# Performance work log

Hardware: AMD Instinct MI355X
Metric: run time of the kernel (lower is better)

## Reference

```python
import jax, jax.numpy as jnp
import numpy as np

NUM_USERS = 50000
NUM_ITEMS = 50000
N_NODES = NUM_USERS + NUM_ITEMS
DIM_FEAT = 256
HID = 128
EMB = 128
K = 3
N_EDGES = 1_600_000


def setup_inputs() -> dict:
    key = jax.random.key(0)
    ks = jax.random.split(key, 16)

    def xavier(k, shape):
        fan_in, fan_out = shape[-2], shape[-1]
        std = float(np.sqrt(2.0 / (fan_in + fan_out)))
        return jax.random.normal(k, shape, dtype=jnp.float32) * std

    return {
        "feat": jax.random.normal(ks[0], (NUM_ITEMS, DIM_FEAT), dtype=jnp.float32),
        "node_emb": jax.random.normal(ks[1], (N_NODES, EMB), dtype=jnp.float32),
        "src": jax.random.randint(ks[2], (N_EDGES,), 0, N_NODES, dtype=jnp.int32),
        "dst": jax.random.randint(ks[3], (N_EDGES,), 0, N_NODES, dtype=jnp.int32),
        "user_feat_emb": xavier(ks[4], (NUM_USERS, HID)),
        "trans_w": xavier(ks[5], (DIM_FEAT, HID)),
        "trans_b": jnp.zeros((HID,), dtype=jnp.float32),
        # layer 0: hidden->hidden; layers 1,2: emb->emb. hidden==emb so stack.
        "ws": xavier(ks[6], (K, HID, HID)),
        "des_w": xavier(ks[7], (K, HID, EMB)),
        "des_b": jnp.zeros((K, EMB), dtype=jnp.float32),
        # concat=True: outs[i] takes [h | u] of width hidden+emb
        "out_w": xavier(ks[8], (K, HID + EMB, EMB)),
        "out_b": jnp.zeros((K, EMB), dtype=jnp.float32),
    }


def reference(feat, node_emb, src, dst, user_feat_emb,
              trans_w, trans_b, ws, des_w, des_b, out_w, out_b):
    # feat = trans(feat); concat user embeddings; L2-normalize rows
    x = feat @ trans_w + trans_b                      # [num_items, HID]
    x = jnp.concatenate([user_feat_emb, x], axis=0)   # [N, HID]
    norm = jnp.linalg.norm(x, axis=1, keepdims=True)
    x = x / jnp.maximum(norm, 1e-12)

    lrelu = jax.nn.leaky_relu  # slope 0.01, matches F.leaky_relu default
    for i in range(K):
        # g.func(x, W): sparse adjacency aggregation (sum over in-edges) then dense W
        agg = jax.ops.segment_sum(x[src], dst, num_segments=N_NODES)  # [N, HID]
        h = lrelu(agg @ ws[i])                                        # [N, HID]
        u = lrelu(h @ des_w[i] + des_b[i] + node_emb)                 # [N, EMB]
        x = lrelu(jnp.concatenate([h, u], axis=1) @ out_w[i] + out_b[i])
    return x, user_feat_emb
```

## Files before the change

### kernel.cpp

```cpp
#include <hip/hip_runtime.h>

#define NN 100000
#define NU 50000
#define NI 50000
#define NE 1600000
#define NSLICE 3
#define SLICEW 33334

#define HSLICE 4
#define HCHUNK 64
#define HSW 25600
#define HEPC (NE/HCHUNK)

typedef unsigned short u16;
typedef unsigned int u32;

typedef __attribute__((ext_vector_type(8))) short s16x8;
typedef __attribute__((ext_vector_type(4))) float f32x4;
typedef __attribute__((ext_vector_type(4))) unsigned short us4;

__device__ __forceinline__ float bf2f(u16 u){
  union { u32 i; float f; } v; v.i = ((u32)u) << 16; return v.f;
}
__device__ __forceinline__ u16 f2bf(float f){
  union { float f; u32 i; } v; v.f = f;
  u32 u = v.i;
  return (u16)((u + 0x7FFFu + ((u >> 16) & 1u)) >> 16);
}
__device__ __forceinline__ u32 pack2(float lo, float hi){
  return (u32)f2bf(lo) | ((u32)f2bf(hi) << 16);
}
__device__ __forceinline__ float lrelu(float x){ return x > 0.f ? x : 0.01f * x; }
__device__ __forceinline__ float san(float v){
  union { float f; u32 i; } u; u.f = v;
  return ((u.i & 0x7F800000u) == 0x7F800000u) ? 0.f : v;
}

__global__ __launch_bounds__(256) void transpose_weights(
    const float* __restrict__ trans_w, const float* __restrict__ wsw,
    const float* __restrict__ desw, const float* __restrict__ outw,
    u16* __restrict__ Ttw, u16* __restrict__ Tw, u16* __restrict__ Td, u16* __restrict__ To)
{
  __shared__ u16 L[128][136];
  int b = blockIdx.x, t = threadIdx.x;
  const float* src; u16* dst; int stride;
  if (b < 2)      { src = trans_w + b*16384;        dst = Ttw + b*128;          stride = 256; }
  else if (b < 5) { int i = b-2; src = wsw  + i*16384; dst = Tw + i*16384;      stride = 128; }
  else if (b < 8) { int i = b-5; src = desw + i*16384; dst = Td + i*16384;      stride = 128; }
  else            { int i = (b-8)>>1, h = (b-8)&1;
                    src = outw + i*32768 + h*16384;    dst = To + i*32768 + h*128; stride = 256; }
  #pragma unroll
  for (int p = 0; p < 8; p++){
    int fi = (p*256 + t)*8;
    int r = fi >> 7, c = fi & 127;
    f32x4 v0 = *(const f32x4*)(src + r*128 + c);
    f32x4 v1 = *(const f32x4*)(src + r*128 + c + 4);
    L[c+0][r] = f2bf(san(v0.x)); L[c+1][r] = f2bf(san(v0.y));
    L[c+2][r] = f2bf(san(v0.z)); L[c+3][r] = f2bf(san(v0.w));
    L[c+4][r] = f2bf(san(v1.x)); L[c+5][r] = f2bf(san(v1.y));
    L[c+6][r] = f2bf(san(v1.z)); L[c+7][r] = f2bf(san(v1.w));
  }
  __syncthreads();
  #pragma unroll
  for (int p = 0; p < 8; p++){
    int fi = (p*256 + t)*8;
    int n = fi >> 7, k = fi & 127;
    us4 o0, o1;
    o0.x = L[n][k+0]; o0.y = L[n][k+1]; o0.z = L[n][k+2]; o0.w = L[n][k+3];
    o1.x = L[n][k+4]; o1.y = L[n][k+5]; o1.z = L[n][k+6]; o1.w = L[n][k+7];
    *(us4*)(dst + (size_t)n*stride + k)     = o0;
    *(us4*)(dst + (size_t)n*stride + k + 4) = o1;
  }
}

__global__ __launch_bounds__(256) void conv_nemb(
    const float* __restrict__ nemb, u16* __restrict__ nembB)
{
  int i = blockIdx.x*256 + threadIdx.x;
  size_t off = (size_t)i * 8;
  f32x4 v0 = *(const f32x4*)(nemb + off);
  f32x4 v1 = *(const f32x4*)(nemb + off + 4);
  us4 o0, o1;
  o0.x = f2bf(san(v0.x)); o0.y = f2bf(san(v0.y)); o0.z = f2bf(san(v0.z)); o0.w = f2bf(san(v0.w));
  o1.x = f2bf(san(v1.x)); o1.y = f2bf(san(v1.y)); o1.z = f2bf(san(v1.z)); o1.w = f2bf(san(v1.w));
  *(us4*)(nembB + off)     = o0;
  *(us4*)(nembB + off + 4) = o1;
}

__global__ __launch_bounds__(256) void norm_users(const float* __restrict__ ufe, u16* __restrict__ X)
{
  int gid = blockIdx.x*256 + threadIdx.x;
  int row = gid >> 6, lane = gid & 63;
  float2 v = *(const float2*)(ufe + (size_t)row*128 + lane*2);
  float a = san(v.x), b = san(v.y);
  float ss = a*a + b*b;
  #pragma unroll
  for (int off = 32; off; off >>= 1) ss += __shfl_xor(ss, off, 64);
  float inv = 1.0f / fmaxf(sqrtf(ss), 1e-12f);
  *(u32*)(X + (size_t)row*128 + lane*2) = pack2(a*inv, b*inv);
}

__global__ __launch_bounds__(256, 4) void trans_items(
    const float* __restrict__ feat, const u16* __restrict__ Ttw,
    const float* __restrict__ tb, u16* __restrict__ X)
{
  __shared__ u16 Af[64][136];
  __shared__ float rowss[64][8];
  __shared__ float rnorm[64];

  int t = threadIdx.x;
  int r0 = blockIdx.x * 64;
  int w = t >> 6, lane = t & 63;
  int l15 = lane & 15, q = lane >> 4;
  int m0 = (w & 1) * 64, n0 = (w >> 1) * 32;

  f32x4 acc[4][2];
  #pragma unroll
  for (int mi = 0; mi < 4; mi++)
    #pragma unroll
    for (int ni = 0; ni < 2; ni++){ acc[mi][ni].x = 0.f; acc[mi][ni].y = 0.f; acc[mi][ni].z = 0.f; acc[mi][ni].w = 0.f; }

  for (int half = 0; half < 2; half++){
    __syncthreads();
    #pragma unroll
    for (int p = 0; p < 4; p++){
      int fi = (p*256 + t)*8;
      int r = fi >> 7, c = fi & 127;
      int row = r0 + r;
      us4 o0 = {0,0,0,0}, o1 = {0,0,0,0};
      if (row < NI){
        f32x4 v0 = *(const f32x4*)(feat + (size_t)row*256 + half*128 + c);
        f32x4 v1 = *(const f32x4*)(feat + (size_t)row*256 + half*128 + c + 4);
        o0.x = f2bf(san(v0.x)); o0.y = f2bf(san(v0.y)); o0.z = f2bf(san(v0.z)); o0.w = f2bf(san(v0.w));
        o1.x = f2bf(san(v1.x)); o1.y = f2bf(san(v1.y)); o1.z = f2bf(san(v1.z)); o1.w = f2bf(san(v1.w));
      }
      *(us4*)&Af[r][c]     = o0;
      *(us4*)&Af[r][c + 4] = o1;
    }
    __syncthreads();
    #pragma unroll
    for (int kc = 0; kc < 128; kc += 32){
      s16x8 afr[4], bfr[2];
      #pragma unroll
      for (int mi = 0; mi < 4; mi++)
        afr[mi] = *(const s16x8*)(Ttw + (size_t)(m0 + 16*mi + l15)*256 + half*128 + kc + 8*q);
      #pragma unroll
      for (int ni = 0; ni < 2; ni++) bfr[ni] = *(const s16x8*)&Af[n0 + 16*ni + l15][kc + 8*q];
      #pragma unroll
      for (int mi = 0; mi < 4; mi++)
        #pragma unroll
        for (int ni = 0; ni < 2; ni++)
          acc[mi][ni] = __builtin_amdgcn_mfma_f32_16x16x32_bf16(afr[mi], bfr[ni], acc[mi][ni], 0, 0, 0);
    }
  }

  float bias[4][4];
  #pragma unroll
  for (int mi = 0; mi < 4; mi++){
    int c0 = m0 + 16*mi + 4*q;
    f32x4 bv = *(const f32x4*)(tb + c0);
    bias[mi][0] = san(bv.x); bias[mi][1] = san(bv.y); bias[mi][2] = san(bv.z); bias[mi][3] = san(bv.w);
  }
  #pragma unroll
  for (int ni = 0; ni < 2; ni++){
    float ss = 0.f;
    #pragma unroll
    for (int mi = 0; mi < 4; mi++){
      float v0 = acc[mi][ni].x + bias[mi][0];
      float v1 = acc[mi][ni].y + bias[mi][1];
      float v2 = acc[mi][ni].z + bias[mi][2];
      float v3 = acc[mi][ni].w + bias[mi][3];
      ss += v0*v0 + v1*v1 + v2*v2 + v3*v3;
    }
    rowss[n0 + 16*ni + l15][(w & 1)*4 + q] = ss;
  }
  __syncthreads();
  if (t < 64){
    float s = 0.f;
    #pragma unroll
    for (int j = 0; j < 8; j++) s += rowss[t][j];
    rnorm[t] = 1.0f / fmaxf(sqrtf(s), 1e-12f);
  }
  __syncthreads();
  #pragma unroll
  for (int mi = 0; mi < 4; mi++){
    int c0 = m0 + 16*mi + 4*q;
    #pragma unroll
    for (int ni = 0; ni < 2; ni++){
      int r = n0 + 16*ni + l15;
      int row = r0 + r;
      if (row < NI){
        float inv = rnorm[r];
        us4 o;
        o.x = f2bf((acc[mi][ni].x + bias[mi][0]) * inv);
        o.y = f2bf((acc[mi][ni].y + bias[mi][1]) * inv);
        o.z = f2bf((acc[mi][ni].z + bias[mi][2]) * inv);
        o.w = f2bf((acc[mi][ni].w + bias[mi][3]) * inv);
        *(us4*)(X + (size_t)(NU + row)*128 + c0) = o;
      }
    }
  }
}

__global__ __launch_bounds__(1024) void hist_lds(
    const int* __restrict__ dst, u32* __restrict__ countsC)
{
  __shared__ u32 cnt[HSW];
  int b = blockIdx.x;
  int s = b / HCHUNK, c = b % HCHUNK;
  int t = threadIdx.x;
  for (int i = t; i < HSW; i += 1024) cnt[i] = 0;
  __syncthreads();
  int lo = s * HSW;
  int hi = min(lo + HSW, NN);
  int e0 = c * HEPC, e1 = e0 + HEPC;
  for (int e = e0 + t*4; e < e1; e += 4096){
    int4 d4 = *(const int4*)(dst + e);
    int d0 = min(max(d4.x, 0), NN-1);
    int d1 = min(max(d4.y, 0), NN-1);
    int d2 = min(max(d4.z, 0), NN-1);
    int d3 = min(max(d4.w, 0), NN-1);
    if (d0 >= lo && d0 < hi) atomicAdd(&cnt[d0 - lo], 1u);
    if (d1 >= lo && d1 < hi) atomicAdd(&cnt[d1 - lo], 1u);
    if (d2 >= lo && d2 < hi) atomicAdd(&cnt[d2 - lo], 1u);
    if (d3 >= lo && d3 < hi) atomicAdd(&cnt[d3 - lo], 1u);
  }
  __syncthreads();
  u32* outp = countsC + (size_t)c*NN + lo;
  int w = hi - lo;
  for (int i = t; i < w; i += 1024) outp[i] = cnt[i];
}

__global__ __launch_bounds__(256) void reduce_counts(
    const u32* __restrict__ countsC, int* __restrict__ counts)
{
  int v = blockIdx.x*256 + threadIdx.x;
  if (v < NN){
    u32 sum = 0;
    #pragma unroll
    for (int c = 0; c < HCHUNK; c++) sum += countsC[(size_t)c*NN + v];
    counts[v] = (int)sum;
  }
}

__global__ __launch_bounds__(1024) void scan_k(const int* __restrict__ counts, int* __restrict__ row_ptr){
  __shared__ int wsum[16];
  __shared__ int woff[16];
  __shared__ int tot;
  int t = threadIdx.x;
  int lane = t & 63, wid = t >> 6;
  int carry = 0;
  for (int base = 0; base < NN; base += 4096){
    int idx = base + t*4;
    int4 v = {0,0,0,0};
    if (idx < NN) v = *(const int4*)(counts + idx);
    int s4 = v.x + v.y + v.z + v.w;
    int s = s4;
    #pragma unroll
    for (int off = 1; off < 64; off <<= 1){
      int u = __shfl_up(s, off, 64);
      if (lane >= off) s += u;
    }
    if (lane == 63) wsum[wid] = s;
    __syncthreads();
    if (t < 16){
      int ws = wsum[t];
      int wscan = ws;
      #pragma unroll
      for (int off = 1; off < 16; off <<= 1){
        int u = __shfl_up(wscan, off, 64);
        if (t >= off) wscan += u;
      }
      woff[t] = wscan - ws;
      if (t == 15) tot = wscan;
    }
    __syncthreads();
    if (idx < NN){
      int e0 = carry + woff[wid] + (s - s4);
      int4 o;
      o.x = e0; o.y = e0 + v.x; o.z = o.y + v.y; o.w = o.z + v.z;
      *(int4*)(row_ptr + idx) = o;
    }
    carry += tot;
    __syncthreads();
  }
}

__global__ __launch_bounds__(256) void fill_slice(
    const int* __restrict__ src, const int* __restrict__ dst,
    int* __restrict__ row_ptr, int* __restrict__ esrc, int d0, int d1)
{
  int e = blockIdx.x*256 + threadIdx.x;
  if (e < NE){
    int d = dst[e];
    if (d >= d0 && d < d1){
      d = min(max(d, 0), NN - 1);
      int pos = atomicAdd(&row_ptr[d], 1);
      pos = min(max(pos, 0), NE - 1);
      esrc[pos] = src[e];
    }
  }
}

#define ACC8(P) \
  a0 += bf2f((u16)(P.x & 0xFFFF)); a1 += bf2f((u16)(P.x >> 16)); \
  a2 += bf2f((u16)(P.y & 0xFFFF)); a3 += bf2f((u16)(P.y >> 16)); \
  a4 += bf2f((u16)(P.z & 0xFFFF)); a5 += bf2f((u16)(P.z >> 16)); \
  a6 += bf2f((u16)(P.w & 0xFFFF)); a7 += bf2f((u16)(P.w >> 16));

__global__ __launch_bounds__(256) void aggregate(
    const u16* __restrict__ X, const int* __restrict__ row_ptr,
    const int* __restrict__ esrc, u16* __restrict__ AGG)
{
  int gid = blockIdx.x*256 + threadIdx.x;
  int v = gid >> 6, lane = gid & 63;
  int sub = lane >> 4, li = lane & 15;
  int jb = (v == 0) ? 0 : row_ptr[v - 1];
  int je = row_ptr[v];
  jb = min(max(jb, 0), NE);
  je = min(max(je, jb), NE);

  float a0=0.f,a1=0.f,a2=0.f,a3=0.f,a4=0.f,a5=0.f,a6=0.f,a7=0.f;

  int j = jb + sub;
  for (; j + 12 < je; j += 16){
    int s0 = esrc[j];      s0 = min(max(s0, 0), NN - 1);
    int s1 = esrc[j + 4];  s1 = min(max(s1, 0), NN - 1);
    int s2 = esrc[j + 8];  s2 = min(max(s2, 0), NN - 1);
    int s3 = esrc[j + 12]; s3 = min(max(s3, 0), NN - 1);
    uint4 p0 = *(const uint4*)(X + (size_t)s0*128 + li*8);
    uint4 p1 = *(const uint4*)(X + (size_t)s1*128 + li*8);
    uint4 p2 = *(const uint4*)(X + (size_t)s2*128 + li*8);
    uint4 p3 = *(const uint4*)(X + (size_t)s3*128 + li*8);
    ACC8(p0); ACC8(p1); ACC8(p2); ACC8(p3);
  }
  for (; j + 4 < je; j += 8){
    int s0 = esrc[j];     s0 = min(max(s0, 0), NN - 1);
    int s1 = esrc[j + 4]; s1 = min(max(s1, 0), NN - 1);
    uint4 p0 = *(const uint4*)(X + (size_t)s0*128 + li*8);
    uint4 p1 = *(const uint4*)(X + (size_t)s1*128 + li*8);
    ACC8(p0); ACC8(p1);
  }
  for (; j < je; j += 4){
    int s0 = esrc[j]; s0 = min(max(s0, 0), NN - 1);
    uint4 p0 = *(const uint4*)(X + (size_t)s0*128 + li*8);
    ACC8(p0);
  }

  a0 += __shfl_xor(a0, 16, 64); a0 += __shfl_xor(a0, 32, 64);
  a1 += __shfl_xor(a1, 16, 64); a1 += __shfl_xor(a1, 32, 64);
  a2 += __shfl_xor(a2, 16, 64); a2 += __shfl_xor(a2, 32, 64);
  a3 += __shfl_xor(a3, 16, 64); a3 += __shfl_xor(a3, 32, 64);
  a4 += __shfl_xor(a4, 16, 64); a4 += __shfl_xor(a4, 32, 64);
  a5 += __shfl_xor(a5, 16, 64); a5 += __shfl_xor(a5, 32, 64);
  a6 += __shfl_xor(a6, 16, 64); a6 += __shfl_xor(a6, 32, 64);
  a7 += __shfl_xor(a7, 16, 64); a7 += __shfl_xor(a7, 32, 64);

  if (sub == 0){
    uint4 o;
    o.x = pack2(a0, a1); o.y = pack2(a2, a3);
    o.z = pack2(a4, a5); o.w = pack2(a6, a7);
    *(uint4*)(AGG + (size_t)v*128 + li*8) = o;
  }
}

__global__ __launch_bounds__(256, 2) void layer_fused(
    const u16* __restrict__ AGG, const u16* __restrict__ nembB,
    const u16* __restrict__ Twi, const u16* __restrict__ Tdi,
    const float* __restrict__ dbF, const u16* __restrict__ Toi,
    const float* __restrict__ obF, u16* __restrict__ XoutB,
    float* __restrict__ XoutF, int last)
{
  __shared__ u16 Ab[128][136];
  __shared__ u16 Hb[128][136];

  int t = threadIdx.x;
  int r0 = blockIdx.x * 128;
  int w = t >> 6, lane = t & 63;
  int l15 = lane & 15, q = lane >> 4;
  int m0 = (w & 1) * 64, n0 = (w >> 1) * 64;

  f32x4 acc[4][4];
  s16x8 wa[4][4], wb[4][4];

#define ZERO_ACC() \
  { _Pragma("unroll") for (int mi = 0; mi < 4; mi++) \
      { _Pragma("unroll") for (int ni = 0; ni < 4; ni++) \
        { acc[mi][ni].x = 0.f; acc[mi][ni].y = 0.f; acc[mi][ni].z = 0.f; acc[mi][ni].w = 0.f; } } }

#define LOADW(WF, WBASE, WSTRIDE, WKOFF) \
  { _Pragma("unroll") for (int mi = 0; mi < 4; mi++) \
      { _Pragma("unroll") for (int kk = 0; kk < 4; kk++) \
          WF[mi][kk] = *(const s16x8*)((WBASE) + (size_t)(m0 + 16*mi + l15)*(WSTRIDE) + (WKOFF) + kk*32 + 8*q); } }

#define MFMA_PHASE(BARR, WF) \
  { _Pragma("unroll") for (int kk = 0; kk < 4; kk++){ \
      s16x8 bfr[4]; \
      _Pragma("unroll") for (int ni = 0; ni < 4; ni++) bfr[ni] = *(const s16x8*)&BARR[n0 + 16*ni + l15][kk*32 + 8*q]; \
      _Pragma("unroll") for (int mi = 0; mi < 4; mi++) \
        { _Pragma("unroll") for (int ni = 0; ni < 4; ni++) \
          acc[mi][ni] = __builtin_amdgcn_mfma_f32_16x16x32_bf16(WF[mi][kk], bfr[ni], acc[mi][ni], 0, 0, 0); } } }

  LOADW(wa, Twi, 128, 0);

  #pragma unroll
  for (int p = 0; p < 8; p++){
    int fi = (p*256 + t)*8;
    int r = fi >> 7, c = fi & 127;
    int row = r0 + r;
    us4 o0 = {0,0,0,0}, o1 = {0,0,0,0};
    if (row < NN){
      o0 = *(const us4*)(AGG + (size_t)row*128 + c);
      o1 = *(const us4*)(AGG + (size_t)row*128 + c + 4);
    }
    *(us4*)&Ab[r][c]     = o0;
    *(us4*)&Ab[r][c + 4] = o1;
  }
  __syncthreads();

  ZERO_ACC();
  LOADW(wb, Tdi, 128, 0);
  MFMA_PHASE(Ab, wa);

  #pragma unroll
  for (int mi = 0; mi < 4; mi++){
    #pragma unroll
    for (int ni = 0; ni < 4; ni++){
      us4 o;
      o.x = f2bf(lrelu(acc[mi][ni].x));
      o.y = f2bf(lrelu(acc[mi][ni].y));
      o.z = f2bf(lrelu(acc[mi][ni].z));
      o.w = f2bf(lrelu(acc[mi][ni].w));
      *(us4*)&Hb[n0 + 16*ni + l15][m0 + 16*mi + 4*q] = o;
    }
  }
  __syncthreads();

  ZERO_ACC();
  LOADW(wa, Toi, 256, 0);
  MFMA_PHASE(Hb, wb);

  #pragma unroll
  for (int mi = 0; mi < 4; mi++){
    int c0 = m0 + 16*mi + 4*q;
    f32x4 dbv = *(const f32x4*)(dbF + c0);
    float db0 = san(dbv.x), db1 = san(dbv.y), db2 = san(dbv.z), db3 = san(dbv.w);
    #pragma unroll
    for (int ni = 0; ni < 4; ni++){
      int r = n0 + 16*ni + l15;
      int row = r0 + r;
      float e0 = 0.f, e1 = 0.f, e2 = 0.f, e3 = 0.f;
      if (row < NN){
        us4 ne = *(const us4*)(nembB + (size_t)row*128 + c0);
        e0 = bf2f(ne.x); e1 = bf2f(ne.y); e2 = bf2f(ne.z); e3 = bf2f(ne.w);
      }
      us4 o;
      o.x = f2bf(lrelu(acc[mi][ni].x + db0 + e0));
      o.y = f2bf(lrelu(acc[mi][ni].y + db1 + e1));
      o.z = f2bf(lrelu(acc[mi][ni].z + db2 + e2));
      o.w = f2bf(lrelu(acc[mi][ni].w + db3 + e3));
      *(us4*)&Ab[r][c0] = o;
    }
  }
  __syncthreads();

  ZERO_ACC();
  LOADW(wb, Toi, 256, 128);
  MFMA_PHASE(Hb, wa);
  MFMA_PHASE(Ab, wb);

  #pragma unroll
  for (int mi = 0; mi < 4; mi++){
    int c0 = m0 + 16*mi + 4*q;
    f32x4 obv = *(const f32x4*)(obF + c0);
    float b0 = san(obv.x), b1 = san(obv.y), b2 = san(obv.z), b3 = san(obv.w);
    #pragma unroll
    for (int ni = 0; ni < 4; ni++){
      int r = n0 + 16*ni + l15;
      int row = r0 + r;
      if (row < NN){
        if (last){
          f32x4 o;
          o.x = lrelu(acc[mi][ni].x + b0);
          o.y = lrelu(acc[mi][ni].y + b1);
          o.z = lrelu(acc[mi][ni].z + b2);
          o.w = lrelu(acc[mi][ni].w + b3);
          *(f32x4*)(XoutF + (size_t)row*128 + c0) = o;
        } else {
          us4 o;
          o.x = f2bf(lrelu(acc[mi][ni].x + b0));
          o.y = f2bf(lrelu(acc[mi][ni].y + b1));
          o.z = f2bf(lrelu(acc[mi][ni].z + b2));
          o.w = f2bf(lrelu(acc[mi][ni].w + b3));
          *(us4*)(XoutB + (size_t)row*128 + c0) = o;
        }
      }
    }
  }
#undef ZERO_ACC
#undef LOADW
#undef MFMA_PHASE
}

__global__ void copy_ufe(const float4* __restrict__ s, float4* __restrict__ d, int n){
  int i = blockIdx.x*256 + threadIdx.x;
  if (i < n){
    float4 v = s[i];
    v.x = san(v.x); v.y = san(v.y); v.z = san(v.z); v.w = san(v.w);
    d[i] = v;
  }
}

extern "C" void kernel_launch(void* const* d_in, const int* in_sizes, int n_in,
                              void* d_out, int out_size, void* d_ws, size_t ws_size,
                              hipStream_t stream)
{
  const float* feat = (const float*)d_in[0];
  const float* nemb = (const float*)d_in[1];
  const int*   src  = (const int*)d_in[2];
  const int*   dst  = (const int*)d_in[3];
  const float* ufe  = (const float*)d_in[4];
  const float* tw   = (const float*)d_in[5];
  const float* tb   = (const float*)d_in[6];
  const float* wsw  = (const float*)d_in[7];
  const float* desw = (const float*)d_in[8];
  const float* desb = (const float*)d_in[9];
  const float* outw = (const float*)d_in[10];
  const float* outb = (const float*)d_in[11];

  float* out  = (float*)d_out;
  float* outU = out + (size_t)NN*128;

  u16* X = (u16*)out;
  u16* nembB = (u16*)outU;

  char* p = (char*)d_ws;
  u16*   AGG = (u16*)p;    p += (size_t)NN*128*2;
  u16*   Ttw = (u16*)p;    p += (size_t)2*16384*2;
  u16*   Tw  = (u16*)p;    p += (size_t)3*16384*2;
  u16*   Td  = (u16*)p;    p += (size_t)3*16384*2;
  u16*   To  = (u16*)p;    p += (size_t)3*32768*2;
  int* row_ptr = (int*)p;  p += (size_t)100004*4;
  int* counts  = (int*)p;  p += (size_t)100000*4;
  int* esrc    = (int*)p;  p += (size_t)NE*4;
  u32* countsC = (u32*)AGG;

  transpose_weights<<<14, 256, 0, stream>>>(tw, wsw, desw, outw, Ttw, Tw, Td, To);
  conv_nemb<<<6250, 256, 0, stream>>>(nemb, nembB);
  norm_users<<<NU/4, 256, 0, stream>>>(ufe, X);
  trans_items<<<(NI + 63)/64, 256, 0, stream>>>(feat, Ttw, tb, X);

  hist_lds<<<HSLICE*HCHUNK, 1024, 0, stream>>>(dst, countsC);
  reduce_counts<<<(NN + 255)/256, 256, 0, stream>>>(countsC, counts);
  scan_k<<<1, 1024, 0, stream>>>(counts, row_ptr);
  for (int s = 0; s < NSLICE; s++){
    fill_slice<<<(NE + 255)/256, 256, 0, stream>>>(src, dst, row_ptr, esrc,
        s*SLICEW, (s == NSLICE-1) ? NN : (s+1)*SLICEW);
  }

  for (int i = 0; i < 3; i++){
    aggregate<<<NN/4, 256, 0, stream>>>(X, row_ptr, esrc, AGG);
    layer_fused<<<(NN + 127)/128, 256, 0, stream>>>(AGG, nembB,
        Tw + (size_t)i*16384, Td + (size_t)i*16384, desb + (size_t)i*128,
        To + (size_t)i*32768, outb + (size_t)i*128, X, out, (i == 2) ? 1 : 0);
  }
  copy_ufe<<<(NU*128/4 + 255)/256, 256, 0, stream>>>((const float4*)ufe, (float4*)outU, NU*128/4);
}
```

Baseline: 713.5 us.

## Fuse CSR gather aggregation into layer GEMM kernel for first two layers

Adds a layer_fused_agg kernel that gathers neighbour rows from the CSR edge list directly into shared memory, then runs the three chained GEMMs. This drops the separate aggregate kernel and the AGG round-trip through global memory for layers 0 and 1, ping-ponging X between buffers. The last layer keeps the separate aggregate path because its output buffer aliases the input. It also stops holding the weight fragments in registers across phases and reloads them per GEMM instead. The fused kernel may lose gather parallelism and latency hiding, since each 16-lane group walks 8 rows serially under a 2-blocks-per-SM launch bound.

```diff
diff --git a/kernel.cpp b/kernel.cpp
--- a/kernel.cpp
+++ b/kernel.cpp
@@ -364,44 +364,158 @@
   }
 }
 
-__global__ __launch_bounds__(256, 2) void layer_fused(
-    const u16* __restrict__ AGG, const u16* __restrict__ nembB,
+#define ZERO_ACC() \
+  { _Pragma("unroll") for (int mi = 0; mi < 4; mi++) \
+      { _Pragma("unroll") for (int ni = 0; ni < 4; ni++) \
+        { acc[mi][ni].x = 0.f; acc[mi][ni].y = 0.f; acc[mi][ni].z = 0.f; acc[mi][ni].w = 0.f; } } }
+
+#define GEMMG(BARR, WBASE, WSTRIDE, WKOFF) \
+  { s16x8 afr[4][4]; \
+    _Pragma("unroll") for (int mi = 0; mi < 4; mi++) \
+      { _Pragma("unroll") for (int kk = 0; kk < 4; kk++) \
+          afr[mi][kk] = *(const s16x8*)((WBASE) + (size_t)(m0 + 16*mi + l15)*(WSTRIDE) + (WKOFF) + kk*32 + 8*q); } \
+    _Pragma("unroll") for (int kk = 0; kk < 4; kk++){ \
+      s16x8 bfr[4]; \
+      _Pragma("unroll") for (int ni = 0; ni < 4; ni++) bfr[ni] = *(const s16x8*)&BARR[n0 + 16*ni + l15][kk*32 + 8*q]; \
+      _Pragma("unroll") for (int mi = 0; mi < 4; mi++) \
+        { _Pragma("unroll") for (int ni = 0; ni < 4; ni++) \
+          acc[mi][ni] = __builtin_amdgcn_mfma_f32_16x16x32_bf16(afr[mi][kk], bfr[ni], acc[mi][ni], 0, 0, 0); } } }
+
+#define LAYER_BODY(NEMBB, TWI, TDI, DBF, TOI, OBF, LAST_EXPR)                  \
+                                                \
+  ZERO_ACC();                                                                  \
+  GEMMG(Ab, TWI, 128, 0);                                                      \
+  _Pragma("unroll")                                                            \
+  for (int mi = 0; mi < 4; mi++){                                              \
+    _Pragma("unroll")                                                          \
+    for (int ni = 0; ni < 4; ni++){                                            \
+      us4 o;                                                                   \
+      o.x = f2bf(lrelu(acc[mi][ni].x));                                        \
+      o.y = f2bf(lrelu(acc[mi][ni].y));                                        \
+      o.z = f2bf(lrelu(acc[mi][ni].z));                                        \
+      o.w = f2bf(lrelu(acc[mi][ni].w));                                        \
+      *(us4*)&Hb[n0 + 16*ni + l15][m0 + 16*mi + 4*q] = o;                      \
+    }                                                                          \
+  }                                                                            \
+  __syncthreads();                                                             \
+                                                  \
+  ZERO_ACC();                                                                  \
+  GEMMG(Hb, TDI, 128, 0);                                                      \
+  _Pragma("unroll")                                                            \
+  for (int mi = 0; mi < 4; mi++){                                              \
+    int c0 = m0 + 16*mi + 4*q;                                                 \
+    f32x4 dbv = *(const f32x4*)(DBF + c0);                                     \
+    float db0 = san(dbv.x), db1 = san(dbv.y), db2 = san(dbv.z), db3 = san(dbv.w); \
+    _Pragma("unroll")                                                          \
+    for (int ni = 0; ni < 4; ni++){                                            \
+      int r = n0 + 16*ni + l15;                                                \
+      int row = r0 + r;                                                        \
+      float e0 = 0.f, e1 = 0.f, e2 = 0.f, e3 = 0.f;                            \
+      if (row < NN){                                                           \
+        us4 ne = *(const us4*)(NEMBB + (size_t)row*128 + c0);                  \
+        e0 = bf2f(ne.x); e1 = bf2f(ne.y); e2 = bf2f(ne.z); e3 = bf2f(ne.w);    \
+      }                                                                        \
+      us4 o;                                                                   \
+      o.x = f2bf(lrelu(acc[mi][ni].x + db0 + e0));                             \
+      o.y = f2bf(lrelu(acc[mi][ni].y + db1 + e1));                             \
+      o.z = f2bf(lrelu(acc[mi][ni].z + db2 + e2));                             \
+      o.w = f2bf(lrelu(acc[mi][ni].w + db3 + e3));                             \
+      *(us4*)&Ab[r][c0] = o;                                                   \
+    }                                                                          \
+  }                                                                            \
+  __syncthreads();                                                             \
+                       \
+  ZERO_ACC();                                                                  \
+  GEMMG(Hb, TOI, 256, 0);                                                      \
+  GEMMG(Ab, TOI, 256, 128);
+
+__global__ __launch_bounds__(256, 2) void layer_fused_agg(
+    const u16* __restrict__ Xin, const int* __restrict__ row_ptr,
+    const int* __restrict__ esrc, const u16* __restrict__ nembB,
     const u16* __restrict__ Twi, const u16* __restrict__ Tdi,
     const float* __restrict__ dbF, const u16* __restrict__ Toi,
-    const float* __restrict__ obF, u16* __restrict__ XoutB,
-    float* __restrict__ XoutF, int last)
-{
-  __shared__ u16 Ab[128][136];
-  __shared__ u16 Hb[128][136];
+    const float* __restrict__ obF, u16* __restrict__ XoutB)
+{
+  __shared__ __align__(16) u16 Ab[128][136];
+  __shared__ __align__(16) u16 Hb[128][136];
 
   int t = threadIdx.x;
   int r0 = blockIdx.x * 128;
   int w = t >> 6, lane = t & 63;
   int l15 = lane & 15, q = lane >> 4;
   int m0 = (w & 1) * 64, n0 = (w >> 1) * 64;
+  int sg = t >> 4, li = t & 15;
 
   f32x4 acc[4][4];
-  s16x8 wa[4][4], wb[4][4];
-
-#define ZERO_ACC() \
-  { _Pragma("unroll") for (int mi = 0; mi < 4; mi++) \
-      { _Pragma("unroll") for (int ni = 0; ni < 4; ni++) \
-        { acc[mi][ni].x = 0.f; acc[mi][ni].y = 0.f; acc[mi][ni].z = 0.f; acc[mi][ni].w = 0.f; } } }
-
-#define LOADW(WF, WBASE, WSTRIDE, WKOFF) \
-  { _Pragma("unroll") for (int mi = 0; mi < 4; mi++) \
-      { _Pragma("unroll") for (int kk = 0; kk < 4; kk++) \
-          WF[mi][kk] = *(const s16x8*)((WBASE) + (size_t)(m0 + 16*mi + l15)*(WSTRIDE) + (WKOFF) + kk*32 + 8*q); } }
-
-#define MFMA_PHASE(BARR, WF) \
-  { _Pragma("unroll") for (int kk = 0; kk < 4; kk++){ \
-      s16x8 bfr[4]; \
-      _Pragma("unroll") for (int ni = 0; ni < 4; ni++) bfr[ni] = *(const s16x8*)&BARR[n0 + 16*ni + l15][kk*32 + 8*q]; \
-      _Pragma("unroll") for (int mi = 0; mi < 4; mi++) \
-        { _Pragma("unroll") for (int ni = 0; ni < 4; ni++) \
-          acc[mi][ni] = __builtin_amdgcn_mfma_f32_16x16x32_bf16(WF[mi][kk], bfr[ni], acc[mi][ni], 0, 0, 0); } } }
-
-  LOADW(wa, Twi, 128, 0);
+
+  for (int k = 0; k < 8; k++){
+    int r = k*16 + sg;
+    int v = r0 + r;
+    float a0=0.f,a1=0.f,a2=0.f,a3=0.f,a4=0.f,a5=0.f,a6=0.f,a7=0.f;
+    if (v < NN){
+      int jb = (v == 0) ? 0 : row_ptr[v - 1];
+      int je = row_ptr[v];
+      jb = min(max(jb, 0), NE);
+      je = min(max(je, jb), NE);
+      for (int j = jb; j < je; j += 8){
+        uint4 pv[8];
+        #pragma unroll
+        for (int i = 0; i < 8; i++){
+          int jj = min(j + i, je - 1);
+          int s = esrc[jj]; s = min(max(s, 0), NN - 1);
+          pv[i] = *(const uint4*)(Xin + (size_t)s*128 + li*8);
+          if (j + i >= je){ pv[i].x = 0u; pv[i].y = 0u; pv[i].z = 0u; pv[i].w = 0u; }
+        }
+        #pragma unroll
+        for (int i = 0; i < 8; i++){ ACC8(pv[i]); }
+      }
+    }
+    uint4 o;
+    o.x = pack2(a0, a1); o.y = pack2(a2, a3);
+    o.z = pack2(a4, a5); o.w = pack2(a6, a7);
+    *(uint4*)&Ab[r][li*8] = o;
+  }
+  __syncthreads();
+
+  LAYER_BODY(nembB, Twi, Tdi, dbF, Toi, obF, 0)
+
+  #pragma unroll
+  for (int mi = 0; mi < 4; mi++){
+    int c0 = m0 + 16*mi + 4*q;
+    f32x4 obv = *(const f32x4*)(obF + c0);
+    float b0 = san(obv.x), b1 = san(obv.y), b2 = san(obv.z), b3 = san(obv.w);
+    #pragma unroll
+    for (int ni = 0; ni < 4; ni++){
+      int r = n0 + 16*ni + l15;
+      int row = r0 + r;
+      if (row < NN){
+        us4 o;
+        o.x = f2bf(lrelu(acc[mi][ni].x + b0));
+        o.y = f2bf(lrelu(acc[mi][ni].y + b1));
+        o.z = f2bf(lrelu(acc[mi][ni].z + b2));
+        o.w = f2bf(lrelu(acc[mi][ni].w + b3));
+        *(us4*)(XoutB + (size_t)row*128 + c0) = o;
+      }
+    }
+  }
+}
+
+__global__ __launch_bounds__(256, 2) void layer_fused(
+    const u16* __restrict__ AGG, const u16* __restrict__ nembB,
+    const u16* __restrict__ Twi, const u16* __restrict__ Tdi,
+    const float* __restrict__ dbF, const u16* __restrict__ Toi,
+    const float* __restrict__ obF, float* __restrict__ XoutF)
+{
+  __shared__ __align__(16) u16 Ab[128][136];
+  __shared__ __align__(16) u16 Hb[128][136];
+
+  int t = threadIdx.x;
+  int r0 = blockIdx.x * 128;
+  int w = t >> 6, lane = t & 63;
+  int l15 = lane & 15, q = lane >> 4;
+  int m0 = (w & 1) * 64, n0 = (w >> 1) * 64;
+
+  f32x4 acc[4][4];
 
   #pragma unroll
   for (int p = 0; p < 8; p++){
@@ -418,56 +532,7 @@
   }
   __syncthreads();
 
-  ZERO_ACC();
-  LOADW(wb, Tdi, 128, 0);
-  MFMA_PHASE(Ab, wa);
-
-  #pragma unroll
-  for (int mi = 0; mi < 4; mi++){
-    #pragma unroll
-    for (int ni = 0; ni < 4; ni++){
-      us4 o;
-      o.x = f2bf(lrelu(acc[mi][ni].x));
-      o.y = f2bf(lrelu(acc[mi][ni].y));
-      o.z = f2bf(lrelu(acc[mi][ni].z));
-      o.w = f2bf(lrelu(acc[mi][ni].w));
-      *(us4*)&Hb[n0 + 16*ni + l15][m0 + 16*mi + 4*q] = o;
-    }
-  }
-  __syncthreads();
-
-  ZERO_ACC();
-  LOADW(wa, Toi, 256, 0);
-  MFMA_PHASE(Hb, wb);
-
-  #pragma unroll
-  for (int mi = 0; mi < 4; mi++){
-    int c0 = m0 + 16*mi + 4*q;
-    f32x4 dbv = *(const f32x4*)(dbF + c0);
-    float db0 = san(dbv.x), db1 = san(dbv.y), db2 = san(dbv.z), db3 = san(dbv.w);
-    #pragma unroll
-    for (int ni = 0; ni < 4; ni++){
-      int r = n0 + 16*ni + l15;
-      int row = r0 + r;
-      float e0 = 0.f, e1 = 0.f, e2 = 0.f, e3 = 0.f;
-      if (row < NN){
-        us4 ne = *(const us4*)(nembB + (size_t)row*128 + c0);
-        e0 = bf2f(ne.x); e1 = bf2f(ne.y); e2 = bf2f(ne.z); e3 = bf2f(ne.w);
-      }
-      us4 o;
-      o.x = f2bf(lrelu(acc[mi][ni].x + db0 + e0));
-      o.y = f2bf(lrelu(acc[mi][ni].y + db1 + e1));
-      o.z = f2bf(lrelu(acc[mi][ni].z + db2 + e2));
-      o.w = f2bf(lrelu(acc[mi][ni].w + db3 + e3));
-      *(us4*)&Ab[r][c0] = o;
-    }
-  }
-  __syncthreads();
-
-  ZERO_ACC();
-  LOADW(wb, Toi, 256, 128);
-  MFMA_PHASE(Hb, wa);
-  MFMA_PHASE(Ab, wb);
+  LAYER_BODY(nembB, Twi, Tdi, dbF, Toi, obF, 1)
 
   #pragma unroll
   for (int mi = 0; mi < 4; mi++){
@@ -479,27 +544,15 @@
       int r = n0 + 16*ni + l15;
       int row = r0 + r;
       if (row < NN){
-        if (last){
-          f32x4 o;
-          o.x = lrelu(acc[mi][ni].x + b0);
-          o.y = lrelu(acc[mi][ni].y + b1);
-          o.z = lrelu(acc[mi][ni].z + b2);
-          o.w = lrelu(acc[mi][ni].w + b3);
-          *(f32x4*)(XoutF + (size_t)row*128 + c0) = o;
-        } else {
-          us4 o;
-          o.x = f2bf(lrelu(acc[mi][ni].x + b0));
-          o.y = f2bf(lrelu(acc[mi][ni].y + b1));
-          o.z = f2bf(lrelu(acc[mi][ni].z + b2));
-          o.w = f2bf(lrelu(acc[mi][ni].w + b3));
-          *(us4*)(XoutB + (size_t)row*128 + c0) = o;
-        }
+        f32x4 o;
+        o.x = lrelu(acc[mi][ni].x + b0);
+        o.y = lrelu(acc[mi][ni].y + b1);
+        o.z = lrelu(acc[mi][ni].z + b2);
+        o.w = lrelu(acc[mi][ni].w + b3);
+        *(f32x4*)(XoutF + (size_t)row*128 + c0) = o;
       }
     }
   }
-#undef ZERO_ACC
-#undef LOADW
-#undef MFMA_PHASE
 }
 
 __global__ void copy_ufe(const float4* __restrict__ s, float4* __restrict__ d, int n){
@@ -544,6 +597,7 @@
   int* counts  = (int*)p;  p += (size_t)100000*4;
   int* esrc    = (int*)p;  p += (size_t)NE*4;
   u32* countsC = (u32*)AGG;
+  u16* X1 = AGG;
 
   transpose_weights<<<14, 256, 0, stream>>>(tw, wsw, desw, outw, Ttw, Tw, Td, To);
   conv_nemb<<<6250, 256, 0, stream>>>(nemb, nembB);
@@ -558,11 +612,14 @@
         s*SLICEW, (s == NSLICE-1) ? NN : (s+1)*SLICEW);
   }
 
-  for (int i = 0; i < 3; i++){
-    aggregate<<<NN/4, 256, 0, stream>>>(X, row_ptr, esrc, AGG);
-    layer_fused<<<(NN + 127)/128, 256, 0, stream>>>(AGG, nembB,
-        Tw + (size_t)i*16384, Td + (size_t)i*16384, desb + (size_t)i*128,
-        To + (size_t)i*32768, outb + (size_t)i*128, X, out, (i == 2) ? 1 : 0);
-  }
+  int nblk = (NN + 127)/128;
+  layer_fused_agg<<<nblk, 256, 0, stream>>>(X, row_ptr, esrc, nembB,
+      Tw, Td, desb, To, outb, X1);
+  layer_fused_agg<<<nblk, 256, 0, stream>>>(X1, row_ptr, esrc, nembB,
+      Tw + 16384, Td + 16384, desb + 128, To + 32768, outb + 128, X);
+  aggregate<<<NN/4, 256, 0, stream>>>(X, row_ptr, esrc, AGG);
+  layer_fused<<<nblk, 256, 0, stream>>>(AGG, nembB,
+      Tw + 2*16384, Td + 2*16384, desb + 2*128, To + 2*32768, outb + 2*128, out);
+
   copy_ufe<<<(NU*128/4 + 255)/256, 256, 0, stream>>>((const float4*)ufe, (float4*)outU, NU*128/4);
 }
```

Measured after the change: 888.3 us. 24.5% more time.
